# Performance work log

Measured on AMD Instinct MI355X. Metric: run time of the kernel, lower is better.

The kernel has to match this reference:

```python
import jax, jax.numpy as jnp
import numpy as np

B, S, H, I, E, TOP_K = 4, 2048, 1024, 4096, 8, 2


def setup_inputs() -> dict:
    key = jax.random.key(0)
    ks = jax.random.split(key, 6)
    x = jax.random.normal(ks[0], (B, S, H), dtype=jnp.float32)
    Wr = jax.random.normal(ks[1], (E, H), dtype=jnp.float32) * 0.02   # router weight (out,in)
    W1 = jax.random.normal(ks[2], (E, I, H), dtype=jnp.float32) * 0.02
    b1 = jnp.zeros((E, I), dtype=jnp.float32)
    W2 = jax.random.normal(ks[3], (E, H, I), dtype=jnp.float32) * 0.02
    b2 = jnp.zeros((E, H), dtype=jnp.float32)
    return {"x": x, "Wr": Wr, "W1": W1, "b1": b1, "W2": W2, "b2": b2}


def reference(x, Wr, W1, b1, W2, b2):
    b, s, h = x.shape
    flat = x.reshape(-1, h)                                   # [T,H]
    logits = jnp.einsum('th,eh->te', flat, Wr)                # [T,E]
    probs = jax.nn.softmax(logits, axis=-1)
    top_p, top_i = jax.lax.top_k(probs, TOP_K)                # [T,K]
    top_p = top_p / jnp.sum(top_p, axis=-1, keepdims=True)
    oh = jax.nn.one_hot(top_i, E, dtype=flat.dtype)           # [T,K,E]
    combine = jnp.einsum('tk,tke->te', top_p, oh)             # [T,E] combine weights
    out = jnp.zeros_like(flat)
    for e in range(E):  # fixed small expert loop (structurally distinct params)
        hidden = jax.nn.gelu(jnp.einsum('th,ih->ti', flat, W1[e]) + b1[e],
                             approximate=False)
        expert_out = jnp.einsum('ti,hi->th', hidden, W2[e]) + b2[e]
        out = out + combine[:, e:e + 1] * expert_out
    # Switch-style aux loss: hard dispatch fraction f vs soft mean prob P
    num_tokens = flat.shape[0]
    counts = jnp.sum(oh, axis=(0, 1))                         # [E]
    f = counts / (num_tokens * TOP_K)
    P = jnp.mean(probs, axis=0)
    aux_loss = E * jnp.sum(f * P)
    return out.reshape(b, s, h), aux_loss
```

## Files before the change

### kernel.cpp

```cpp
#include <hip/hip_runtime.h>
#include <hip/hip_bf16.h>
#include <cstdint>
#include <cstddef>

#define T_TOK 8192
#define H_DIM 1024
#define I_DIM 4096
#define E_NUM 8
#define NSLOT (T_TOK*2)
#define ROUTER_BLOCKS 512

#define OFF_CNT     0
#define OFF_PSUM    1024
#define OFF_GATE    32768
#define OFF_ROWMAP  131072
#define OFF_XB      (1ull<<20)
#define OFF_Y       (1ull<<20)
#define OFF_WB1     (17ull<<20)
#define OFF_WB2     (81ull<<20)
#define OFF_HID     (145ull<<20)

typedef __attribute__((ext_vector_type(8))) short bf16x8;
typedef __attribute__((ext_vector_type(4))) float f32x4;

__device__ __forceinline__ void gll16(const void* g, void* l) {
    __builtin_amdgcn_global_load_lds((const __attribute__((address_space(1))) void*)g,
                                     (__attribute__((address_space(3))) void*)l, 16, 0, 0);
}

__device__ __forceinline__ ushort f2bf(float f) {
    uint32_t u = __float_as_uint(f);
    return (ushort)((u + 0x7FFFu + ((u >> 16) & 1u)) >> 16);
}

__global__ void init_kernel(int* __restrict__ cnt) {
    if (threadIdx.x < E_NUM) cnt[threadIdx.x] = 0;
}

__global__ __launch_bounds__(256) void f2bf_kernel(const float* __restrict__ s,
                                                   ushort* __restrict__ d, int n4) {
    for (int i = blockIdx.x * 256 + threadIdx.x; i < n4; i += gridDim.x * 256) {
        const float4 v = ((const float4*)s)[i];
        ushort4 o;
        o.x = f2bf(v.x); o.y = f2bf(v.y); o.z = f2bf(v.z); o.w = f2bf(v.w);
        ((ushort4*)d)[i] = o;
    }
}

__global__ __launch_bounds__(256) void router_kernel(
    const float* __restrict__ x, const float* __restrict__ Wr,
    int* __restrict__ cnt, float* __restrict__ psum_part,
    float* __restrict__ gate, int* __restrict__ rowmap)
{
    __shared__ float ps[E_NUM];
    __shared__ int   lcnt[E_NUM];
    __shared__ int   lbase[E_NUM];
    const int tid  = threadIdx.x;
    const int lane = tid & 63;
    const int wid  = tid >> 6;
    if (tid < E_NUM) { ps[tid] = 0.0f; lcnt[tid] = 0; }
    __syncthreads();

    int   e_idx[4][2];
    int   e_pos[4][2];
    float e_w[4][2];

#pragma unroll
    for (int it = 0; it < 4; ++it) {
        const int t = blockIdx.x * 16 + wid * 4 + it;
        const float* xr = x + (size_t)t * H_DIM;
        float xv[16];
#pragma unroll
        for (int j = 0; j < 16; ++j) xv[j] = xr[lane + j * 64];
        float l[E_NUM];
#pragma unroll
        for (int e = 0; e < E_NUM; ++e) {
            const float* wr = Wr + e * H_DIM;
            float s = 0.0f;
#pragma unroll
            for (int j = 0; j < 16; ++j) s += xv[j] * wr[lane + j * 64];
#pragma unroll
            for (int off = 32; off > 0; off >>= 1) s += __shfl_xor(s, off, 64);
            l[e] = s;
        }
        float m = l[0];
#pragma unroll
        for (int e = 1; e < E_NUM; ++e) m = fmaxf(m, l[e]);
        float p[E_NUM], sum = 0.0f;
#pragma unroll
        for (int e = 0; e < E_NUM; ++e) { p[e] = expf(l[e] - m); sum += p[e]; }
        const float inv = 1.0f / sum;
#pragma unroll
        for (int e = 0; e < E_NUM; ++e) p[e] *= inv;
        int i0 = 0;
#pragma unroll
        for (int e = 1; e < E_NUM; ++e) if (p[e] > p[i0]) i0 = e;
        int i1 = (i0 == 0) ? 1 : 0;
#pragma unroll
        for (int e = 0; e < E_NUM; ++e) if (e != i0 && p[e] > p[i1]) i1 = e;
        const float s2 = p[i0] + p[i1];

        if (lane == 0) {
            e_idx[it][0] = i0; e_idx[it][1] = i1;
            e_w[it][0] = p[i0] / s2; e_w[it][1] = p[i1] / s2;
            e_pos[it][0] = atomicAdd(&lcnt[i0], 1);
            e_pos[it][1] = atomicAdd(&lcnt[i1], 1);
#pragma unroll
            for (int e = 0; e < E_NUM; ++e) atomicAdd(&ps[e], p[e]);
        }
    }
    __syncthreads();
    if (tid < E_NUM) {
        lbase[tid] = atomicAdd(&cnt[tid], lcnt[tid]);
        psum_part[blockIdx.x * E_NUM + tid] = ps[tid];
    }
    __syncthreads();
    if (lane == 0) {
#pragma unroll
        for (int it = 0; it < 4; ++it) {
            const int t = blockIdx.x * 16 + wid * 4 + it;
#pragma unroll
            for (int k = 0; k < 2; ++k) {
                const int e = e_idx[it][k];
                const int pos = lbase[e] + e_pos[it][k];
                rowmap[e * T_TOK + pos] = 2 * t + k;
                gate[2 * t + k] = e_w[it][k];
            }
        }
    }
}

template<int N, int K, bool FIRST>
__global__ __launch_bounds__(256) void moe_gemm_mfma(
    const ushort* __restrict__ A,
    const ushort* __restrict__ W,
    const float* __restrict__ bias,
    ushort* __restrict__ OutBf,
    float* __restrict__ OutF,
    const int* __restrict__ rowmap,
    const int* __restrict__ cnt)
{
    const int e  = blockIdx.z;
    const int cnt_e = cnt[e];
    const int row0 = blockIdx.y * 128;
    if (row0 >= cnt_e) return;
    const int col0 = blockIdx.x * 128;

    __shared__ int    sslot[128];
    __shared__ ushort lA[128 * 32];
    __shared__ ushort lB[128 * 32];

    const int tid = threadIdx.x, lane = tid & 63, w = tid >> 6;
    if (tid < 128) {
        const int r = row0 + tid;
        sslot[tid] = (r < cnt_e) ? rowmap[e * T_TOK + r] : -1;
    }
    __syncthreads();

    const int rsub = lane >> 2;
    const int s4   = lane & 3;
    const ushort* gA[2]; const ushort* gB[2];
    ushort* ldA[2]; ushort* ldB[2];
#pragma unroll
    for (int c = 0; c < 2; ++c) {
        const int r = (w * 2 + c) * 16 + rsub;
        const int g = s4 ^ ((r >> 1) & 3);
        int srow = sslot[r]; if (srow < 0) srow = 0;
        const int arow = FIRST ? (srow >> 1) : srow;
        gA[c]  = A + (size_t)arow * K + g * 8;
        gB[c]  = W + ((size_t)e * N + col0 + r) * K + g * 8;
        ldA[c] = &lA[(w * 2 + c) * 512];
        ldB[c] = &lB[(w * 2 + c) * 512];
    }

    const int fr = lane & 15;
    const int kq = lane >> 4;
    int offA[4], offB[4];
#pragma unroll
    for (int i = 0; i < 4; ++i) {
        const int r  = (w >> 1) * 64 + i * 16 + fr;
        offA[i] = r * 32 + (kq ^ ((r >> 1) & 3)) * 8;
        const int cr = (w & 1) * 64 + i * 16 + fr;
        offB[i] = cr * 32 + (kq ^ ((cr >> 1) & 3)) * 8;
    }

    f32x4 acc[4][4] = {};
    for (int kt = 0; kt < K; kt += 32) {
#pragma unroll
        for (int c = 0; c < 2; ++c) {
            gll16(gA[c] + kt, ldA[c]);
            gll16(gB[c] + kt, ldB[c]);
        }
        __syncthreads();
        bf16x8 af[4], bfr[4];
#pragma unroll
        for (int i = 0; i < 4; ++i) {
            af[i]  = *(const bf16x8*)&lA[offA[i]];
            bfr[i] = *(const bf16x8*)&lB[offB[i]];
        }
#pragma unroll
        for (int mi = 0; mi < 4; ++mi)
#pragma unroll
            for (int ni = 0; ni < 4; ++ni)
                acc[mi][ni] = __builtin_amdgcn_mfma_f32_16x16x32_bf16(
                    af[mi], bfr[ni], acc[mi][ni], 0, 0, 0);
        __syncthreads();
    }

    const int wrb = (w >> 1) * 64, wcb = (w & 1) * 64;
    float bb[4];
#pragma unroll
    for (int ni = 0; ni < 4; ++ni) bb[ni] = bias[e * N + col0 + wcb + ni * 16 + fr];
    const int rowhi = lane >> 4;
#pragma unroll
    for (int mi = 0; mi < 4; ++mi) {
#pragma unroll
        for (int j = 0; j < 4; ++j) {
            const int r = wrb + mi * 16 + rowhi * 4 + j;
            if (row0 + r < cnt_e) {
                const int slot = sslot[r];
#pragma unroll
                for (int ni = 0; ni < 4; ++ni) {
                    const int cg = col0 + wcb + ni * 16 + fr;
                    float v = acc[mi][ni][j] + bb[ni];
                    if (FIRST) {
                        v = 0.5f * v * (1.0f + erff(v * 0.70710678118654752f));
                        OutBf[(size_t)slot * N + cg] = f2bf(v);
                    } else {
                        OutF[(size_t)slot * N + cg] = v;
                    }
                }
            }
        }
    }
}

__global__ __launch_bounds__(256) void combine_kernel(
    const float* __restrict__ y, const float* __restrict__ gate,
    float* __restrict__ out)
{
    const int i  = blockIdx.x * blockDim.x + threadIdx.x;
    const int t  = i >> 8;
    const int hq = (i & 255) * 4;
    const float w0 = gate[2 * t];
    const float w1 = gate[2 * t + 1];
    const float4 a = *(const float4*)(y + (size_t)(2 * t) * H_DIM + hq);
    const float4 b = *(const float4*)(y + (size_t)(2 * t + 1) * H_DIM + hq);
    float4 o;
    o.x = w0 * a.x + w1 * b.x;
    o.y = w0 * a.y + w1 * b.y;
    o.z = w0 * a.z + w1 * b.z;
    o.w = w0 * a.w + w1 * b.w;
    *(float4*)(out + (size_t)t * H_DIM + hq) = o;
}

__global__ void finalize_kernel(const int* __restrict__ cnt,
                                const float* __restrict__ psum_part,
                                float* __restrict__ out_aux)
{
    __shared__ float P[E_NUM];
    __shared__ float F[E_NUM];
    if (threadIdx.x < E_NUM) {
        float s = 0.0f;
        for (int b = 0; b < ROUTER_BLOCKS; ++b) s += psum_part[b * E_NUM + threadIdx.x];
        P[threadIdx.x] = s / (float)T_TOK;
        F[threadIdx.x] = (float)cnt[threadIdx.x] / (float)(T_TOK * 2);
    }
    __syncthreads();
    if (threadIdx.x == 0) {
        float a = 0.0f;
        for (int e = 0; e < E_NUM; ++e) a += F[e] * P[e];
        out_aux[0] = (float)E_NUM * a;
    }
}

extern "C" void kernel_launch(void* const* d_in, const int* in_sizes, int n_in,
                              void* d_out, int out_size, void* d_ws, size_t ws_size,
                              hipStream_t stream)
{
    const float* x  = (const float*)d_in[0];
    const float* Wr = (const float*)d_in[1];
    const float* W1 = (const float*)d_in[2];
    const float* b1 = (const float*)d_in[3];
    const float* W2 = (const float*)d_in[4];
    const float* b2 = (const float*)d_in[5];
    float* out = (float*)d_out;

    char* ws = (char*)d_ws;
    int*    cnt    = (int*)(ws + OFF_CNT);
    float*  psum   = (float*)(ws + OFF_PSUM);
    float*  gate   = (float*)(ws + OFF_GATE);
    int*    rowmap = (int*)(ws + OFF_ROWMAP);
    ushort* xb     = (ushort*)(ws + OFF_XB);
    ushort* wb1    = (ushort*)(ws + OFF_WB1);
    ushort* wb2    = (ushort*)(ws + OFF_WB2);
    ushort* hid    = (ushort*)(ws + OFF_HID);
    float*  yb     = (float*)(ws + OFF_Y);

    hipLaunchKernelGGL(init_kernel, dim3(1), dim3(64), 0, stream, cnt);
    hipLaunchKernelGGL(router_kernel, dim3(ROUTER_BLOCKS), dim3(256), 0, stream,
                       x, Wr, cnt, psum, gate, rowmap);
    hipLaunchKernelGGL(f2bf_kernel, dim3(2048), dim3(256), 0, stream,
                       x, xb, T_TOK * H_DIM / 4);
    hipLaunchKernelGGL(f2bf_kernel, dim3(2048), dim3(256), 0, stream,
                       W1, wb1, E_NUM * I_DIM * H_DIM / 4);
    hipLaunchKernelGGL(f2bf_kernel, dim3(2048), dim3(256), 0, stream,
                       W2, wb2, E_NUM * H_DIM * I_DIM / 4);
    hipLaunchKernelGGL((moe_gemm_mfma<I_DIM, H_DIM, true>),
                       dim3(I_DIM / 128, T_TOK / 128, E_NUM), dim3(256), 0, stream,
                       xb, wb1, b1, hid, nullptr, rowmap, cnt);
    hipLaunchKernelGGL((moe_gemm_mfma<H_DIM, I_DIM, false>),
                       dim3(H_DIM / 128, T_TOK / 128, E_NUM), dim3(256), 0, stream,
                       hid, wb2, b2, nullptr, yb, rowmap, cnt);
    hipLaunchKernelGGL(combine_kernel, dim3((T_TOK * H_DIM / 4) / 256), dim3(256), 0, stream,
                       yb, gate, out);
    hipLaunchKernelGGL(finalize_kernel, dim3(1), dim3(64), 0, stream,
                       cnt, psum, out + (size_t)T_TOK * H_DIM);
}
```

Before: 920.7 us.

## Double-buffer MoE GEMM LDS, compact block list, fuse x cast and combine via atomics

```diff
diff --git a/kernel.cpp b/kernel.cpp
--- a/kernel.cpp
+++ b/kernel.cpp
@@ -9,13 +9,16 @@
 #define E_NUM 8
 #define NSLOT (T_TOK*2)
 #define ROUTER_BLOCKS 512
+#define MAXBLK 144
 
 #define OFF_CNT     0
-#define OFF_PSUM    1024
+#define OFF_NBLK    128
+#define OFF_BLKE    256
+#define OFF_BLKRB   1024
+#define OFF_PSUM    2048
 #define OFF_GATE    32768
 #define OFF_ROWMAP  131072
 #define OFF_XB      (1ull<<20)
-#define OFF_Y       (1ull<<20)
 #define OFF_WB1     (17ull<<20)
 #define OFF_WB2     (81ull<<20)
 #define OFF_HID     (145ull<<20)
@@ -47,10 +50,16 @@
     }
 }
 
+__global__ __launch_bounds__(256) void zero_out_kernel(float* __restrict__ out) {
+    const int i = blockIdx.x * 256 + threadIdx.x;
+    ((float4*)out)[i] = make_float4(0.f, 0.f, 0.f, 0.f);
+}
+
 __global__ __launch_bounds__(256) void router_kernel(
     const float* __restrict__ x, const float* __restrict__ Wr,
     int* __restrict__ cnt, float* __restrict__ psum_part,
-    float* __restrict__ gate, int* __restrict__ rowmap)
+    float* __restrict__ gate, int* __restrict__ rowmap,
+    ushort* __restrict__ xb)
 {
     __shared__ float ps[E_NUM];
     __shared__ int   lcnt[E_NUM];
@@ -72,6 +81,8 @@
         float xv[16];
 #pragma unroll
         for (int j = 0; j < 16; ++j) xv[j] = xr[lane + j * 64];
+#pragma unroll
+        for (int j = 0; j < 16; ++j) xb[(size_t)t * H_DIM + lane + j * 64] = f2bf(xv[j]);
         float l[E_NUM];
 #pragma unroll
         for (int e = 0; e < E_NUM; ++e) {
@@ -130,25 +141,41 @@
     }
 }
 
+__global__ void blocklist_kernel(const int* __restrict__ cnt, int* __restrict__ nblk,
+                                 int* __restrict__ be, int* __restrict__ brb) {
+    if (threadIdx.x == 0) {
+        int nb = 0;
+        for (int e = 0; e < E_NUM; ++e) {
+            const int nrb = (cnt[e] + 127) >> 7;
+            for (int rb = 0; rb < nrb; ++rb) { be[nb] = e; brb[nb] = rb; ++nb; }
+        }
+        nblk[0] = nb;
+    }
+}
+
 template<int N, int K, bool FIRST>
 __global__ __launch_bounds__(256) void moe_gemm_mfma(
     const ushort* __restrict__ A,
     const ushort* __restrict__ W,
     const float* __restrict__ bias,
     ushort* __restrict__ OutBf,
-    float* __restrict__ OutF,
+    float* __restrict__ OutAcc,
+    const float* __restrict__ gate,
     const int* __restrict__ rowmap,
-    const int* __restrict__ cnt)
+    const int* __restrict__ cnt,
+    const int* __restrict__ nblk,
+    const int* __restrict__ blk_e,
+    const int* __restrict__ blk_rb)
 {
-    const int e  = blockIdx.z;
+    const int by = blockIdx.y;
+    if (by >= nblk[0]) return;
+    const int e = blk_e[by];
     const int cnt_e = cnt[e];
-    const int row0 = blockIdx.y * 128;
-    if (row0 >= cnt_e) return;
+    const int row0 = blk_rb[by] * 128;
     const int col0 = blockIdx.x * 128;
 
     __shared__ int    sslot[128];
-    __shared__ ushort lA[128 * 32];
-    __shared__ ushort lB[128 * 32];
+    __shared__ ushort lds[2][2][128 * 32];
 
     const int tid = threadIdx.x, lane = tid & 63, w = tid >> 6;
     if (tid < 128) {
@@ -160,7 +187,7 @@
     const int rsub = lane >> 2;
     const int s4   = lane & 3;
     const ushort* gA[2]; const ushort* gB[2];
-    ushort* ldA[2]; ushort* ldB[2];
+    int ldoff[2];
 #pragma unroll
     for (int c = 0; c < 2; ++c) {
         const int r = (w * 2 + c) * 16 + rsub;
@@ -169,8 +196,7 @@
         const int arow = FIRST ? (srow >> 1) : srow;
         gA[c]  = A + (size_t)arow * K + g * 8;
         gB[c]  = W + ((size_t)e * N + col0 + r) * K + g * 8;
-        ldA[c] = &lA[(w * 2 + c) * 512];
-        ldB[c] = &lB[(w * 2 + c) * 512];
+        ldoff[c] = (w * 2 + c) * 512;
     }
 
     const int fr = lane & 15;
@@ -185,18 +211,28 @@
     }
 
     f32x4 acc[4][4] = {};
-    for (int kt = 0; kt < K; kt += 32) {
-#pragma unroll
-        for (int c = 0; c < 2; ++c) {
-            gll16(gA[c] + kt, ldA[c]);
-            gll16(gB[c] + kt, ldB[c]);
-        }
-        __syncthreads();
+
+#pragma unroll
+    for (int c = 0; c < 2; ++c) {
+        gll16(gA[c], &lds[0][0][ldoff[c]]);
+        gll16(gB[c], &lds[0][1][ldoff[c]]);
+    }
+    __syncthreads();
+
+    int cur = 0;
+    for (int kt = 32; kt <= K; kt += 32) {
+        if (kt < K) {
+#pragma unroll
+            for (int c = 0; c < 2; ++c) {
+                gll16(gA[c] + kt, &lds[cur ^ 1][0][ldoff[c]]);
+                gll16(gB[c] + kt, &lds[cur ^ 1][1][ldoff[c]]);
+            }
+        }
         bf16x8 af[4], bfr[4];
 #pragma unroll
         for (int i = 0; i < 4; ++i) {
-            af[i]  = *(const bf16x8*)&lA[offA[i]];
-            bfr[i] = *(const bf16x8*)&lB[offB[i]];
+            af[i]  = *(const bf16x8*)&lds[cur][0][offA[i]];
+            bfr[i] = *(const bf16x8*)&lds[cur][1][offB[i]];
         }
 #pragma unroll
         for (int mi = 0; mi < 4; ++mi)
@@ -205,6 +241,7 @@
                 acc[mi][ni] = __builtin_amdgcn_mfma_f32_16x16x32_bf16(
                     af[mi], bfr[ni], acc[mi][ni], 0, 0, 0);
         __syncthreads();
+        cur ^= 1;
     }
 
     const int wrb = (w >> 1) * 64, wcb = (w & 1) * 64;
@@ -219,39 +256,26 @@
             const int r = wrb + mi * 16 + rowhi * 4 + j;
             if (row0 + r < cnt_e) {
                 const int slot = sslot[r];
-#pragma unroll
-                for (int ni = 0; ni < 4; ++ni) {
-                    const int cg = col0 + wcb + ni * 16 + fr;
-                    float v = acc[mi][ni][j] + bb[ni];
-                    if (FIRST) {
+                if (FIRST) {
+#pragma unroll
+                    for (int ni = 0; ni < 4; ++ni) {
+                        const int cg = col0 + wcb + ni * 16 + fr;
+                        float v = acc[mi][ni][j] + bb[ni];
                         v = 0.5f * v * (1.0f + erff(v * 0.70710678118654752f));
                         OutBf[(size_t)slot * N + cg] = f2bf(v);
-                    } else {
-                        OutF[(size_t)slot * N + cg] = v;
+                    }
+                } else {
+                    const float gw = gate[slot];
+                    float* op = OutAcc + (size_t)(slot >> 1) * H_DIM;
+#pragma unroll
+                    for (int ni = 0; ni < 4; ++ni) {
+                        const int cg = col0 + wcb + ni * 16 + fr;
+                        atomicAdd(op + cg, gw * (acc[mi][ni][j] + bb[ni]));
                     }
                 }
             }
         }
     }
-}
-
-__global__ __launch_bounds__(256) void combine_kernel(
-    const float* __restrict__ y, const float* __restrict__ gate,
-    float* __restrict__ out)
-{
-    const int i  = blockIdx.x * blockDim.x + threadIdx.x;
-    const int t  = i >> 8;
-    const int hq = (i & 255) * 4;
-    const float w0 = gate[2 * t];
-    const float w1 = gate[2 * t + 1];
-    const float4 a = *(const float4*)(y + (size_t)(2 * t) * H_DIM + hq);
-    const float4 b = *(const float4*)(y + (size_t)(2 * t + 1) * H_DIM + hq);
-    float4 o;
-    o.x = w0 * a.x + w1 * b.x;
-    o.y = w0 * a.y + w1 * b.y;
-    o.z = w0 * a.z + w1 * b.z;
-    o.w = w0 * a.w + w1 * b.w;
-    *(float4*)(out + (size_t)t * H_DIM + hq) = o;
 }
 
 __global__ void finalize_kernel(const int* __restrict__ cnt,
@@ -288,6 +312,9 @@
 
     char* ws = (char*)d_ws;
     int*    cnt    = (int*)(ws + OFF_CNT);
+    int*    nblk   = (int*)(ws + OFF_NBLK);
+    int*    blke   = (int*)(ws + OFF_BLKE);
+    int*    blkrb  = (int*)(ws + OFF_BLKRB);
     float*  psum   = (float*)(ws + OFF_PSUM);
     float*  gate   = (float*)(ws + OFF_GATE);
     int*    rowmap = (int*)(ws + OFF_ROWMAP);
@@ -295,25 +322,24 @@
     ushort* wb1    = (ushort*)(ws + OFF_WB1);
     ushort* wb2    = (ushort*)(ws + OFF_WB2);
     ushort* hid    = (ushort*)(ws + OFF_HID);
-    float*  yb     = (float*)(ws + OFF_Y);
 
     hipLaunchKernelGGL(init_kernel, dim3(1), dim3(64), 0, stream, cnt);
     hipLaunchKernelGGL(router_kernel, dim3(ROUTER_BLOCKS), dim3(256), 0, stream,
-                       x, Wr, cnt, psum, gate, rowmap);
-    hipLaunchKernelGGL(f2bf_kernel, dim3(2048), dim3(256), 0, stream,
-                       x, xb, T_TOK * H_DIM / 4);
+                       x, Wr, cnt, psum, gate, rowmap, xb);
+    hipLaunchKernelGGL(blocklist_kernel, dim3(1), dim3(64), 0, stream,
+                       cnt, nblk, blke, blkrb);
     hipLaunchKernelGGL(f2bf_kernel, dim3(2048), dim3(256), 0, stream,
                        W1, wb1, E_NUM * I_DIM * H_DIM / 4);
     hipLaunchKernelGGL(f2bf_kernel, dim3(2048), dim3(256), 0, stream,
                        W2, wb2, E_NUM * H_DIM * I_DIM / 4);
+    hipLaunchKernelGGL(zero_out_kernel, dim3(T_TOK * H_DIM / 4 / 256), dim3(256), 0, stream,
+                       out);
     hipLaunchKernelGGL((moe_gemm_mfma<I_DIM, H_DIM, true>),
-                       dim3(I_DIM / 128, T_TOK / 128, E_NUM), dim3(256), 0, stream,
-                       xb, wb1, b1, hid, nullptr, rowmap, cnt);
+                       dim3(I_DIM / 128, MAXBLK), dim3(256), 0, stream,
+                       xb, wb1, b1, hid, nullptr, gate, rowmap, cnt, nblk, blke, blkrb);
     hipLaunchKernelGGL((moe_gemm_mfma<H_DIM, I_DIM, false>),
-                       dim3(H_DIM / 128, T_TOK / 128, E_NUM), dim3(256), 0, stream,
-                       hid, wb2, b2, nullptr, yb, rowmap, cnt);
-    hipLaunchKernelGGL(combine_kernel, dim3((T_TOK * H_DIM / 4) / 256), dim3(256), 0, stream,
-                       yb, gate, out);
+                       dim3(H_DIM / 128, MAXBLK), dim3(256), 0, stream,
+                       hid, wb2, b2, nullptr, out, gate, rowmap, cnt, nblk, blke, blkrb);
     hipLaunchKernelGGL(finalize_kernel, dim3(1), dim3(64), 0, stream,
                        cnt, psum, out + (size_t)T_TOK * H_DIM);
 }
```

Result: slower. 961.7 us (+4.5%).
